# Optimization experiments

Measured on AMD Instinct MI355X. Metric: run time of the kernel, lower is better.

## Reference

```python
import jax, jax.numpy as jnp
import numpy as np

B, T, E, H, D = 4, 2048, 1024, 16, 64


def setup_inputs() -> dict:
    key = jax.random.key(0)
    k1, k2, k3, k4 = jax.random.split(key, 4)
    s = 1.0 / np.sqrt(E)
    return {
        "x": jax.random.normal(k1, (B, T, E), dtype=jnp.float32),
        "wj_w": jax.random.uniform(k2, (E, E), jnp.float32, -s, s),   # torch Linear weight (out,in)
        "wjv_w": jax.random.uniform(k3, (E, E), jnp.float32, -s, s),
        "wo_w": jax.random.uniform(k4, (E, H * D), jnp.float32, -s, s),
    }


def reference(x, wj_w, wjv_w, wo_w):
    b, t, e = x.shape
    # echo = x @ wj_w.T ; eb = echo @ wj_w  (F.linear with transposed weight)
    eb = (x @ wj_w.T) @ wj_w
    sc = jnp.sum(x * eb, axis=-1) / jnp.sqrt(jnp.asarray(e, x.dtype))  # (B,T)
    # rank-1 outer-product scores with strict-upper causal mask
    ja = sc[:, :, None] * sc[:, None, :]                               # (B,T,T)
    causal = jnp.tril(jnp.ones((t, t), dtype=bool))
    ja = jnp.where(causal[None], ja, -jnp.inf)
    ja = jax.nn.softmax(ja, axis=-1)                                   # (B,T,T)
    # values per head; attention map shared across heads (broadcast, not materialized)
    val = (x @ wjv_w.T).reshape(b, t, H, D)                            # (B,T,H,D)
    out = jnp.einsum("bts,bshd->bthd", ja, val)                       # (B,T,H,D)
    return out.reshape(b, t, H * D) @ wo_w.T                           # (B,T,E)
```

## Files before the change

kernel.cpp:

```cpp
#include <hip/hip_runtime.h>
#include <math.h>

#define R_ROWS 8192
#define T_SEQ  2048
#define E_DIM  1024

typedef __attribute__((ext_vector_type(8))) short short8;
typedef __attribute__((ext_vector_type(4))) float f32x4;

__device__ __forceinline__ ushort f2bf(float f) {
  uint u = __float_as_uint(f);
  u += 0x7FFFu + ((u >> 16) & 1u);
  return (ushort)(u >> 16);
}
__device__ __forceinline__ float bf2f(ushort h) {
  return __uint_as_float(((uint)h) << 16);
}

__global__ __launch_bounds__(256) void cvt_bf16(
    const float* __restrict__ in, ushort* __restrict__ out, int n4)
{
  int i = blockIdx.x * 256 + threadIdx.x;
  if (i >= n4) return;
  float4 v = ((const float4*)in)[i];
  ushort4 o;
  o.x = f2bf(v.x); o.y = f2bf(v.y); o.z = f2bf(v.z); o.w = f2bf(v.w);
  ((ushort4*)out)[i] = o;
}

__global__ __launch_bounds__(256) void cvt_split(
    const float* __restrict__ in, ushort* __restrict__ hi,
    ushort* __restrict__ lo, int n4)
{
  int i = blockIdx.x * 256 + threadIdx.x;
  if (i >= n4) return;
  float4 v = ((const float4*)in)[i];
  ushort4 h, l;
  h.x = f2bf(v.x); l.x = f2bf(v.x - bf2f(h.x));
  h.y = f2bf(v.y); l.y = f2bf(v.y - bf2f(h.y));
  h.z = f2bf(v.z); l.z = f2bf(v.z - bf2f(h.z));
  h.w = f2bf(v.w); l.w = f2bf(v.w - bf2f(h.w));
  ((ushort4*)hi)[i] = h;
  ((ushort4*)lo)[i] = l;
}

__global__ __launch_bounds__(256) void gemm_sq_split(
    const ushort* __restrict__ xh, const ushort* __restrict__ xl,
    const ushort* __restrict__ wh, const ushort* __restrict__ wl,
    float* __restrict__ sc_raw)
{
  const int K = 1024;
  __shared__ ushort Ah[128][40];
  __shared__ ushort Al[128][40];
  __shared__ ushort Bh[128][40];
  __shared__ ushort Bl[128][40];
  const int tid = threadIdx.x;
  const int m0 = blockIdx.y * 128, n0 = blockIdx.x * 128;
  const int wave = tid >> 6, lane = tid & 63;
  const int l15 = lane & 15, lq = lane >> 4;
  const int wm = (wave & 1) * 64, wn = (wave >> 1) * 64;
  const int srow = tid >> 2, scol = (tid & 3) * 8;

  f32x4 acc[4][4] = {};
  const ushort* xhp = xh + (size_t)(m0 + srow) * K + scol;
  const ushort* xlp = xl + (size_t)(m0 + srow) * K + scol;
  const ushort* whp = wh + (size_t)(n0 + srow) * K + scol;
  const ushort* wlp = wl + (size_t)(n0 + srow) * K + scol;

  for (int k0 = 0; k0 < K; k0 += 32) {
    const uint4 ah0 = *(const uint4*)(xhp + k0);
    const uint4 ah1 = *(const uint4*)(xhp + (size_t)64*K + k0);
    const uint4 al0 = *(const uint4*)(xlp + k0);
    const uint4 al1 = *(const uint4*)(xlp + (size_t)64*K + k0);
    const uint4 bh0 = *(const uint4*)(whp + k0);
    const uint4 bh1 = *(const uint4*)(whp + (size_t)64*K + k0);
    const uint4 bl0 = *(const uint4*)(wlp + k0);
    const uint4 bl1 = *(const uint4*)(wlp + (size_t)64*K + k0);
    __syncthreads();
    *(uint4*)&Ah[srow][scol] = ah0;  *(uint4*)&Ah[srow+64][scol] = ah1;
    *(uint4*)&Al[srow][scol] = al0;  *(uint4*)&Al[srow+64][scol] = al1;
    *(uint4*)&Bh[srow][scol] = bh0;  *(uint4*)&Bh[srow+64][scol] = bh1;
    *(uint4*)&Bl[srow][scol] = bl0;  *(uint4*)&Bl[srow+64][scol] = bl1;
    __syncthreads();
    short8 bhf[4], blf[4];
#pragma unroll
    for (int j = 0; j < 4; ++j) {
      bhf[j] = *(const short8*)&Bh[wn + j*16 + l15][lq*8];
      blf[j] = *(const short8*)&Bl[wn + j*16 + l15][lq*8];
    }
#pragma unroll
    for (int i = 0; i < 4; ++i) {
      const short8 ahf = *(const short8*)&Ah[wm + i*16 + l15][lq*8];
      const short8 alf = *(const short8*)&Al[wm + i*16 + l15][lq*8];
#pragma unroll
      for (int j = 0; j < 4; ++j) {
        acc[i][j] = __builtin_amdgcn_mfma_f32_16x16x32_bf16(ahf, bhf[j], acc[i][j], 0, 0, 0);
        acc[i][j] = __builtin_amdgcn_mfma_f32_16x16x32_bf16(ahf, blf[j], acc[i][j], 0, 0, 0);
        acc[i][j] = __builtin_amdgcn_mfma_f32_16x16x32_bf16(alf, bhf[j], acc[i][j], 0, 0, 0);
      }
    }
  }

  __syncthreads();
  float* red = (float*)&Ah[0][0];
#pragma unroll
  for (int i = 0; i < 4; ++i)
#pragma unroll
    for (int r = 0; r < 4; ++r) {
      const int row = wm + i*16 + lq*4 + r;
      float s = 0.f;
#pragma unroll
      for (int j = 0; j < 4; ++j) s += acc[i][j][r] * acc[i][j][r];
      red[row*33 + (wave>>1)*16 + l15] = s;
    }
  __syncthreads();
  if (tid < 128) {
    float s = 0.f;
#pragma unroll
    for (int c = 0; c < 32; ++c) s += red[tid*33 + c];
    atomicAdd(&sc_raw[m0 + tid], s);
  }
}

__global__ __launch_bounds__(1024) void scan_max(
    const float* __restrict__ sc_raw, float* __restrict__ sc,
    float* __restrict__ pmax)
{
  const int b = blockIdx.x;
  __shared__ float b0[T_SEQ];
  __shared__ float b1[T_SEQ];
  const int tid = threadIdx.x;
  for (int i = tid; i < T_SEQ; i += 1024) {
    const float v = sc_raw[b*T_SEQ + i] * 0.03125f;
    b0[i] = v;
    sc[b*T_SEQ + i] = v;
  }
  __syncthreads();
  float* src = b0; float* dst = b1;
  for (int off = 1; off < T_SEQ; off <<= 1) {
    for (int i = tid; i < T_SEQ; i += 1024)
      dst[i] = (i >= off) ? fmaxf(src[i], src[i - off]) : src[i];
    __syncthreads();
    float* tmp = src; src = dst; dst = tmp;
  }
  for (int i = tid; i < T_SEQ; i += 1024) pmax[b*T_SEQ + i] = src[i];
}

template<bool OUT_BF16>
__global__ __launch_bounds__(256) void gemm_bf16(
    const ushort* __restrict__ A, const ushort* __restrict__ B,
    void* __restrict__ Cout, int M, int N, int K)
{
  __shared__ ushort As[128][40];
  __shared__ ushort Bs[128][40];
  const int tid = threadIdx.x;
  const int m0 = blockIdx.y * 128, n0 = blockIdx.x * 128;
  const int wave = tid >> 6, lane = tid & 63;
  const int l15 = lane & 15, lq = lane >> 4;
  const int wm = (wave & 1) * 64, wn = (wave >> 1) * 64;
  const int srow = tid >> 2, scol = (tid & 3) * 8;

  f32x4 acc[4][4] = {};
  const ushort* Ap = A + (size_t)(m0 + srow) * K + scol;
  const ushort* Bp = B + (size_t)(n0 + srow) * K + scol;

  for (int k0 = 0; k0 < K; k0 += 32) {
    const uint4 a0 = *(const uint4*)(Ap + k0);
    const uint4 a1 = *(const uint4*)(Ap + (size_t)64 * K + k0);
    const uint4 b0 = *(const uint4*)(Bp + k0);
    const uint4 b1 = *(const uint4*)(Bp + (size_t)64 * K + k0);
    __syncthreads();
    *(uint4*)&As[srow     ][scol] = a0;
    *(uint4*)&As[srow + 64][scol] = a1;
    *(uint4*)&Bs[srow     ][scol] = b0;
    *(uint4*)&Bs[srow + 64][scol] = b1;
    __syncthreads();
    short8 af[4], bfr[4];
#pragma unroll
    for (int i = 0; i < 4; ++i)
      af[i] = *(const short8*)&As[wm + i*16 + l15][lq*8];
#pragma unroll
    for (int j = 0; j < 4; ++j)
      bfr[j] = *(const short8*)&Bs[wn + j*16 + l15][lq*8];
#pragma unroll
    for (int i = 0; i < 4; ++i)
#pragma unroll
      for (int j = 0; j < 4; ++j)
        acc[i][j] = __builtin_amdgcn_mfma_f32_16x16x32_bf16(af[i], bfr[j], acc[i][j], 0, 0, 0);
  }

#pragma unroll
  for (int i = 0; i < 4; ++i)
#pragma unroll
    for (int j = 0; j < 4; ++j) {
      const int mb = m0 + wm + i*16 + lq*4;
      const int nb = n0 + wn + j*16 + l15;
#pragma unroll
      for (int r = 0; r < 4; ++r) {
        if (OUT_BF16)
          ((ushort*)Cout)[(size_t)(mb + r) * N + nb] = f2bf(acc[i][j][r]);
        else
          ((float*)Cout)[(size_t)(mb + r) * N + nb] = acc[i][j][r];
      }
    }
}

__global__ __launch_bounds__(512) void attn_mfma(
    const ushort* __restrict__ valT, const float* __restrict__ sc,
    const float* __restrict__ pmax, ushort* __restrict__ attnN)
{
  __shared__ float scs_all[T_SEQ];
  __shared__ ushort p[2][128][72];
  __shared__ float zsh[128][4];
  __shared__ float zinv[128];

  const int b  = blockIdx.z;
  const int e0 = blockIdx.x * 128;
  const int tid = threadIdx.x;
  const int wave = tid >> 6, lane = tid & 63;
  const int l15 = lane & 15, lq = lane >> 4;
  const int wm = (wave & 1) * 64;
  const int wn = (wave >> 1) * 32;
  const int bT = b * T_SEQ;

  *(float4*)&scs_all[tid * 4] = *(const float4*)&sc[bT + tid * 4];
  __syncthreads();

  const int prow = tid >> 2;
  const int pc = (tid & 3) * 16;

#pragma unroll 1
  for (int ph = 0; ph < 2; ++ph) {
    const int ty = ph == 0 ? (15 - (int)blockIdx.y) : (int)blockIdx.y;
    const int t0 = ty * 128;
    const int nchunk = 2 * ty + 2;

    const int tglob = t0 + prow;
    const float st = sc[bT + tglob];
    const float pm = pmax[bT + tglob];

    f32x4 acc[4][2] = {};
    float zp = 0.f;

    auto pgen = [&](int c, int buf) -> float {
      const int s0 = c * 64;
      float sv[16];
#pragma unroll
      for (int q = 0; q < 4; ++q)
        *(float4*)&sv[q*4] = *(const float4*)&scs_all[s0 + pc + q*4];
      ushort tmp[16];
      float z = 0.f;
#pragma unroll
      for (int k = 0; k < 16; ++k) {
        const int sg = s0 + pc + k;
        float pe = 0.f;
        if (sg <= tglob) pe = __expf(st * (sv[k] - pm));
        const ushort h = f2bf(pe);
        tmp[k] = h;
        z += bf2f(h);
      }
      *(uint4*)&p[buf][prow][pc    ] = *(const uint4*)&tmp[0];
      *(uint4*)&p[buf][prow][pc + 8] = *(const uint4*)&tmp[8];
      return z;
    };

    auto loadB = [&](short8* dst, int c) {
#pragma unroll
      for (int j = 0; j < 2; ++j)
#pragma unroll
        for (int ksi = 0; ksi < 2; ++ksi)
          dst[j*2 + ksi] = *(const short8*)&valT[
              (size_t)(e0 + wn + j*16 + l15) * R_ROWS + bT + c*64 + ksi*32 + lq*8];
    };

    auto mstep = [&](int buf, const short8* bfr) {
#pragma unroll
      for (int ksi = 0; ksi < 2; ++ksi) {
        short8 af[4];
#pragma unroll
        for (int i = 0; i < 4; ++i)
          af[i] = *(const short8*)&p[buf][wm + i*16 + l15][ksi*32 + lq*8];
#pragma unroll
        for (int i = 0; i < 4; ++i)
#pragma unroll
          for (int j = 0; j < 2; ++j)
            acc[i][j] = __builtin_amdgcn_mfma_f32_16x16x32_bf16(
                af[i], bfr[j*2 + ksi], acc[i][j], 0, 0, 0);
      }
    };

    short8 bA[4], bB[4];
    zp += pgen(0, 0);
    loadB(bA, 0);
    __syncthreads();

#pragma unroll 1
    for (int c = 0; c < nchunk; ++c) {
      if ((c & 1) == 0) {
        if (c + 1 < nchunk) { loadB(bB, c + 1); zp += pgen(c + 1, 1); }
        mstep(0, bA);
      } else {
        if (c + 1 < nchunk) { loadB(bA, c + 1); zp += pgen(c + 1, 0); }
        mstep(1, bB);
      }
      __syncthreads();
    }

    zsh[prow][tid & 3] = zp;
    __syncthreads();
    if (tid < 128)
      zinv[tid] = 1.0f / (zsh[tid][0] + zsh[tid][1] + zsh[tid][2] + zsh[tid][3]);
    __syncthreads();

#pragma unroll
    for (int i = 0; i < 4; ++i)
#pragma unroll
      for (int j = 0; j < 2; ++j) {
        const int nb = e0 + wn + j*16 + l15;
#pragma unroll
        for (int r = 0; r < 4; ++r) {
          const int ml = wm + i*16 + lq*4 + r;
          const float v = acc[i][j][r] * zinv[ml];
          attnN[(size_t)(bT + t0 + ml) * E_DIM + nb] = f2bf(v);
        }
      }
    __syncthreads();
  }
}

extern "C" void kernel_launch(void* const* d_in, const int* in_sizes, int n_in,
                              void* d_out, int out_size, void* d_ws, size_t ws_size,
                              hipStream_t stream) {
  (void)in_sizes; (void)n_in; (void)out_size; (void)ws_size;
  const float* x   = (const float*)d_in[0];
  const float* wj  = (const float*)d_in[1];
  const float* wjv = (const float*)d_in[2];
  const float* wo  = (const float*)d_in[3];
  float* out = (float*)d_out;

  ushort* xh    = (ushort*)d_ws;
  ushort* xl    = xh    + (size_t)R_ROWS * E_DIM;
  ushort* wjh   = xl    + (size_t)R_ROWS * E_DIM;
  ushort* wjl   = wjh   + (size_t)E_DIM * E_DIM;
  ushort* wjvb  = wjl   + (size_t)E_DIM * E_DIM;
  ushort* wob   = wjvb  + (size_t)E_DIM * E_DIM;
  ushort* valT  = wob   + (size_t)E_DIM * E_DIM;
  float* sc_raw = (float*)(valT + (size_t)E_DIM * R_ROWS);
  float* sc     = sc_raw + R_ROWS;
  float* pmax   = sc + R_ROWS;
  ushort* attnN = xl;

  hipMemsetAsync(sc_raw, 0, R_ROWS * sizeof(float), stream);

  cvt_split<<<R_ROWS*E_DIM/4/256, 256, 0, stream>>>(x,  xh,  xl,  R_ROWS*E_DIM/4);
  cvt_split<<<E_DIM*E_DIM/4/256, 256, 0, stream>>>(wj, wjh, wjl, E_DIM*E_DIM/4);
  cvt_bf16<<<E_DIM*E_DIM/4/256, 256, 0, stream>>>(wjv, wjvb, E_DIM*E_DIM/4);
  cvt_bf16<<<E_DIM*E_DIM/4/256, 256, 0, stream>>>(wo,  wob,  E_DIM*E_DIM/4);

  gemm_sq_split<<<dim3(E_DIM/128, R_ROWS/128), 256, 0, stream>>>(
      xh, xl, wjh, wjl, sc_raw);
  scan_max<<<4, 1024, 0, stream>>>(sc_raw, sc, pmax);

  gemm_bf16<true><<<dim3(R_ROWS/128, E_DIM/128), 256, 0, stream>>>(
      wjvb, xh, valT, E_DIM, R_ROWS, E_DIM);

  attn_mfma<<<dim3(E_DIM/128, 8, 4), 512, 0, stream>>>(valT, sc, pmax, attnN);

  gemm_bf16<false><<<dim3(E_DIM/128, R_ROWS/128), 256, 0, stream>>>(
      attnN, wob, out, R_ROWS, E_DIM, E_DIM);
}
```

Baseline: 277.8 us.

## Pre-swizzle operands into MFMA fragment layout and load GEMM fragments directly from global

```diff
diff --git a/kernel.cpp b/kernel.cpp
--- a/kernel.cpp
+++ b/kernel.cpp
@@ -4,6 +4,7 @@
 #define R_ROWS 8192
 #define T_SEQ  2048
 #define E_DIM  1024
+#define KC     32
 
 typedef __attribute__((ext_vector_type(8))) short short8;
 typedef __attribute__((ext_vector_type(4))) float f32x4;
@@ -15,6 +16,48 @@
 }
 __device__ __forceinline__ float bf2f(ushort h) {
   return __uint_as_float(((uint)h) << 16);
+}
+
+
+__global__ __launch_bounds__(256) void cvt_split_frag(
+    const float* __restrict__ in, ushort* __restrict__ hi,
+    ushort* __restrict__ lo, int n)
+{
+  int g = blockIdx.x * 256 + threadIdx.x;
+  if (g >= n) return;
+  const int l = g & 15, h = (g >> 4) & 3;
+  const int pq = g >> 6;
+  const int q = pq & (KC - 1), p = pq >> 5;
+  const size_t src = (size_t)(p * 16 + l) * 1024 + q * 32 + h * 8;
+  const float4 v0 = *(const float4*)&in[src];
+  const float4 v1 = *(const float4*)&in[src + 4];
+  ushort hh[8], ll[8];
+  const float v[8] = {v0.x, v0.y, v0.z, v0.w, v1.x, v1.y, v1.z, v1.w};
+#pragma unroll
+  for (int e = 0; e < 8; ++e) {
+    hh[e] = f2bf(v[e]);
+    ll[e] = f2bf(v[e] - bf2f(hh[e]));
+  }
+  *(uint4*)&hi[(size_t)g * 8] = *(const uint4*)hh;
+  *(uint4*)&lo[(size_t)g * 8] = *(const uint4*)ll;
+}
+
+__global__ __launch_bounds__(256) void cvt_bf16_frag(
+    const float* __restrict__ in, ushort* __restrict__ out, int n)
+{
+  int g = blockIdx.x * 256 + threadIdx.x;
+  if (g >= n) return;
+  const int l = g & 15, h = (g >> 4) & 3;
+  const int pq = g >> 6;
+  const int q = pq & (KC - 1), p = pq >> 5;
+  const size_t src = (size_t)(p * 16 + l) * 1024 + q * 32 + h * 8;
+  const float4 v0 = *(const float4*)&in[src];
+  const float4 v1 = *(const float4*)&in[src + 4];
+  ushort hh[8];
+  const float v[8] = {v0.x, v0.y, v0.z, v0.w, v1.x, v1.y, v1.z, v1.w};
+#pragma unroll
+  for (int e = 0; e < 8; ++e) hh[e] = f2bf(v[e]);
+  *(uint4*)&out[(size_t)g * 8] = *(const uint4*)hh;
 }
 
 __global__ __launch_bounds__(256) void cvt_bf16(
@@ -28,96 +71,79 @@
   ((ushort4*)out)[i] = o;
 }
 
-__global__ __launch_bounds__(256) void cvt_split(
-    const float* __restrict__ in, ushort* __restrict__ hi,
-    ushort* __restrict__ lo, int n4)
-{
-  int i = blockIdx.x * 256 + threadIdx.x;
-  if (i >= n4) return;
-  float4 v = ((const float4*)in)[i];
-  ushort4 h, l;
-  h.x = f2bf(v.x); l.x = f2bf(v.x - bf2f(h.x));
-  h.y = f2bf(v.y); l.y = f2bf(v.y - bf2f(h.y));
-  h.z = f2bf(v.z); l.z = f2bf(v.z - bf2f(h.z));
-  h.w = f2bf(v.w); l.w = f2bf(v.w - bf2f(h.w));
-  ((ushort4*)hi)[i] = h;
-  ((ushort4*)lo)[i] = l;
-}
-
-__global__ __launch_bounds__(256) void gemm_sq_split(
+struct Frags { short8 ah[4], al[4], bh[4], bl[4]; };
+
+__global__ __launch_bounds__(256, 2) void gemm_sq_direct(
     const ushort* __restrict__ xh, const ushort* __restrict__ xl,
     const ushort* __restrict__ wh, const ushort* __restrict__ wl,
     float* __restrict__ sc_raw)
 {
-  const int K = 1024;
-  __shared__ ushort Ah[128][40];
-  __shared__ ushort Al[128][40];
-  __shared__ ushort Bh[128][40];
-  __shared__ ushort Bl[128][40];
   const int tid = threadIdx.x;
   const int m0 = blockIdx.y * 128, n0 = blockIdx.x * 128;
   const int wave = tid >> 6, lane = tid & 63;
   const int l15 = lane & 15, lq = lane >> 4;
   const int wm = (wave & 1) * 64, wn = (wave >> 1) * 64;
-  const int srow = tid >> 2, scol = (tid & 3) * 8;
+
+  size_t aoff[4], boff[4];
+#pragma unroll
+  for (int i = 0; i < 4; ++i)
+    aoff[i] = ((size_t)(((m0 + wm) >> 4) + i) * KC * 4 + lq) * 128 + l15 * 8;
+#pragma unroll
+  for (int j = 0; j < 4; ++j)
+    boff[j] = ((size_t)(((n0 + wn) >> 4) + j) * KC * 4 + lq) * 128 + l15 * 8;
 
   f32x4 acc[4][4] = {};
-  const ushort* xhp = xh + (size_t)(m0 + srow) * K + scol;
-  const ushort* xlp = xl + (size_t)(m0 + srow) * K + scol;
-  const ushort* whp = wh + (size_t)(n0 + srow) * K + scol;
-  const ushort* wlp = wl + (size_t)(n0 + srow) * K + scol;
-
-  for (int k0 = 0; k0 < K; k0 += 32) {
-    const uint4 ah0 = *(const uint4*)(xhp + k0);
-    const uint4 ah1 = *(const uint4*)(xhp + (size_t)64*K + k0);
-    const uint4 al0 = *(const uint4*)(xlp + k0);
-    const uint4 al1 = *(const uint4*)(xlp + (size_t)64*K + k0);
-    const uint4 bh0 = *(const uint4*)(whp + k0);
-    const uint4 bh1 = *(const uint4*)(whp + (size_t)64*K + k0);
-    const uint4 bl0 = *(const uint4*)(wlp + k0);
-    const uint4 bl1 = *(const uint4*)(wlp + (size_t)64*K + k0);
-    __syncthreads();
-    *(uint4*)&Ah[srow][scol] = ah0;  *(uint4*)&Ah[srow+64][scol] = ah1;
-    *(uint4*)&Al[srow][scol] = al0;  *(uint4*)&Al[srow+64][scol] = al1;
-    *(uint4*)&Bh[srow][scol] = bh0;  *(uint4*)&Bh[srow+64][scol] = bh1;
-    *(uint4*)&Bl[srow][scol] = bl0;  *(uint4*)&Bl[srow+64][scol] = bl1;
-    __syncthreads();
-    short8 bhf[4], blf[4];
+  Frags f0, f1;
+
+  auto load = [&](Frags& f, int q) {
+    const size_t dq = (size_t)q * 512;
+#pragma unroll
+    for (int i = 0; i < 4; ++i) {
+      f.ah[i] = *(const short8*)(xh + aoff[i] + dq);
+      f.al[i] = *(const short8*)(xl + aoff[i] + dq);
+    }
 #pragma unroll
     for (int j = 0; j < 4; ++j) {
-      bhf[j] = *(const short8*)&Bh[wn + j*16 + l15][lq*8];
-      blf[j] = *(const short8*)&Bl[wn + j*16 + l15][lq*8];
-    }
-#pragma unroll
-    for (int i = 0; i < 4; ++i) {
-      const short8 ahf = *(const short8*)&Ah[wm + i*16 + l15][lq*8];
-      const short8 alf = *(const short8*)&Al[wm + i*16 + l15][lq*8];
+      f.bh[j] = *(const short8*)(wh + boff[j] + dq);
+      f.bl[j] = *(const short8*)(wl + boff[j] + dq);
+    }
+  };
+  auto step = [&](const Frags& f) {
+#pragma unroll
+    for (int i = 0; i < 4; ++i)
 #pragma unroll
       for (int j = 0; j < 4; ++j) {
-        acc[i][j] = __builtin_amdgcn_mfma_f32_16x16x32_bf16(ahf, bhf[j], acc[i][j], 0, 0, 0);
-        acc[i][j] = __builtin_amdgcn_mfma_f32_16x16x32_bf16(ahf, blf[j], acc[i][j], 0, 0, 0);
-        acc[i][j] = __builtin_amdgcn_mfma_f32_16x16x32_bf16(alf, bhf[j], acc[i][j], 0, 0, 0);
-      }
-    }
-  }
-
-  __syncthreads();
-  float* red = (float*)&Ah[0][0];
+        acc[i][j] = __builtin_amdgcn_mfma_f32_16x16x32_bf16(f.ah[i], f.bh[j], acc[i][j], 0, 0, 0);
+        acc[i][j] = __builtin_amdgcn_mfma_f32_16x16x32_bf16(f.ah[i], f.bl[j], acc[i][j], 0, 0, 0);
+        acc[i][j] = __builtin_amdgcn_mfma_f32_16x16x32_bf16(f.al[i], f.bh[j], acc[i][j], 0, 0, 0);
+      }
+  };
+
+  load(f0, 0);
+#pragma unroll 1
+  for (int q = 0; q < KC; q += 2) {
+    load(f1, q + 1);
+    step(f0);
+    if (q + 2 < KC) load(f0, q + 2);
+    step(f1);
+  }
+
+  __shared__ float red[128][33];
 #pragma unroll
   for (int i = 0; i < 4; ++i)
 #pragma unroll
     for (int r = 0; r < 4; ++r) {
-      const int row = wm + i*16 + lq*4 + r;
+      const int row = wm + i * 16 + lq * 4 + r;
       float s = 0.f;
 #pragma unroll
       for (int j = 0; j < 4; ++j) s += acc[i][j][r] * acc[i][j][r];
-      red[row*33 + (wave>>1)*16 + l15] = s;
+      red[row][(l15 << 1) | (wave >> 1)] = s;
     }
   __syncthreads();
   if (tid < 128) {
     float s = 0.f;
 #pragma unroll
-    for (int c = 0; c < 32; ++c) s += red[tid*33 + c];
+    for (int c = 0; c < 32; ++c) s += red[tid][c];
     atomicAdd(&sc_raw[m0 + tid], s);
   }
 }
@@ -147,41 +173,41 @@
 }
 
 template<bool OUT_BF16>
-__global__ __launch_bounds__(256) void gemm_bf16(
-    const ushort* __restrict__ A, const ushort* __restrict__ B,
-    void* __restrict__ Cout, int M, int N, int K)
+__global__ __launch_bounds__(256) void gemm_bf16_bfrag(
+    const ushort* __restrict__ A, const ushort* __restrict__ Bf,
+    void* __restrict__ Cout, int N, int K)
 {
   __shared__ ushort As[128][40];
-  __shared__ ushort Bs[128][40];
   const int tid = threadIdx.x;
   const int m0 = blockIdx.y * 128, n0 = blockIdx.x * 128;
   const int wave = tid >> 6, lane = tid & 63;
   const int l15 = lane & 15, lq = lane >> 4;
   const int wm = (wave & 1) * 64, wn = (wave >> 1) * 64;
   const int srow = tid >> 2, scol = (tid & 3) * 8;
+  const int Kc = K >> 5;
 
   f32x4 acc[4][4] = {};
   const ushort* Ap = A + (size_t)(m0 + srow) * K + scol;
-  const ushort* Bp = B + (size_t)(n0 + srow) * K + scol;
-
-  for (int k0 = 0; k0 < K; k0 += 32) {
-    const uint4 a0 = *(const uint4*)(Ap + k0);
-    const uint4 a1 = *(const uint4*)(Ap + (size_t)64 * K + k0);
-    const uint4 b0 = *(const uint4*)(Bp + k0);
-    const uint4 b1 = *(const uint4*)(Bp + (size_t)64 * K + k0);
+  size_t boff[4];
+#pragma unroll
+  for (int j = 0; j < 4; ++j)
+    boff[j] = ((size_t)(((n0 + wn) >> 4) + j) * Kc * 4 + lq) * 128 + l15 * 8;
+
+  for (int q = 0; q < Kc; ++q) {
+    const uint4 a0 = *(const uint4*)(Ap + q * 32);
+    const uint4 a1 = *(const uint4*)(Ap + (size_t)64 * K + q * 32);
+    short8 bfr[4];
+#pragma unroll
+    for (int j = 0; j < 4; ++j)
+      bfr[j] = *(const short8*)(Bf + boff[j] + (size_t)q * 512);
     __syncthreads();
     *(uint4*)&As[srow     ][scol] = a0;
     *(uint4*)&As[srow + 64][scol] = a1;
-    *(uint4*)&Bs[srow     ][scol] = b0;
-    *(uint4*)&Bs[srow + 64][scol] = b1;
-    __syncthreads();
-    short8 af[4], bfr[4];
+    __syncthreads();
+    short8 af[4];
 #pragma unroll
     for (int i = 0; i < 4; ++i)
       af[i] = *(const short8*)&As[wm + i*16 + l15][lq*8];
-#pragma unroll
-    for (int j = 0; j < 4; ++j)
-      bfr[j] = *(const short8*)&Bs[wn + j*16 + l15][lq*8];
 #pragma unroll
     for (int i = 0; i < 4; ++i)
 #pragma unroll
@@ -338,34 +364,34 @@
   const float* wo  = (const float*)d_in[3];
   float* out = (float*)d_out;
 
-  ushort* xh    = (ushort*)d_ws;
-  ushort* xl    = xh    + (size_t)R_ROWS * E_DIM;
-  ushort* wjh   = xl    + (size_t)R_ROWS * E_DIM;
-  ushort* wjl   = wjh   + (size_t)E_DIM * E_DIM;
-  ushort* wjvb  = wjl   + (size_t)E_DIM * E_DIM;
-  ushort* wob   = wjvb  + (size_t)E_DIM * E_DIM;
-  ushort* valT  = wob   + (size_t)E_DIM * E_DIM;
-  float* sc_raw = (float*)(valT + (size_t)E_DIM * R_ROWS);
+  ushort* xh_f  = (ushort*)d_ws;
+  ushort* xl_f  = xh_f  + (size_t)R_ROWS * E_DIM;
+  ushort* wjh_f = xl_f  + (size_t)R_ROWS * E_DIM;
+  ushort* wjl_f = wjh_f + (size_t)E_DIM * E_DIM;
+  ushort* wjvb  = wjl_f + (size_t)E_DIM * E_DIM;
+  ushort* wob_f = wjvb  + (size_t)E_DIM * E_DIM;
+  float* sc_raw = (float*)(wob_f + (size_t)E_DIM * E_DIM);
   float* sc     = sc_raw + R_ROWS;
   float* pmax   = sc + R_ROWS;
-  ushort* attnN = xl;
+  ushort* valT  = xl_f;
+  ushort* attnN = xh_f;
 
   hipMemsetAsync(sc_raw, 0, R_ROWS * sizeof(float), stream);
 
-  cvt_split<<<R_ROWS*E_DIM/4/256, 256, 0, stream>>>(x,  xh,  xl,  R_ROWS*E_DIM/4);
-  cvt_split<<<E_DIM*E_DIM/4/256, 256, 0, stream>>>(wj, wjh, wjl, E_DIM*E_DIM/4);
+  cvt_split_frag<<<R_ROWS*E_DIM/8/256, 256, 0, stream>>>(x,  xh_f,  xl_f,  R_ROWS*E_DIM/8);
+  cvt_split_frag<<<E_DIM*E_DIM/8/256, 256, 0, stream>>>(wj, wjh_f, wjl_f, E_DIM*E_DIM/8);
   cvt_bf16<<<E_DIM*E_DIM/4/256, 256, 0, stream>>>(wjv, wjvb, E_DIM*E_DIM/4);
-  cvt_bf16<<<E_DIM*E_DIM/4/256, 256, 0, stream>>>(wo,  wob,  E_DIM*E_DIM/4);
-
-  gemm_sq_split<<<dim3(E_DIM/128, R_ROWS/128), 256, 0, stream>>>(
-      xh, xl, wjh, wjl, sc_raw);
+  cvt_bf16_frag<<<E_DIM*E_DIM/8/256, 256, 0, stream>>>(wo, wob_f, E_DIM*E_DIM/8);
+
+  gemm_sq_direct<<<dim3(E_DIM/128, R_ROWS/128), 256, 0, stream>>>(
+      xh_f, xl_f, wjh_f, wjl_f, sc_raw);
   scan_max<<<4, 1024, 0, stream>>>(sc_raw, sc, pmax);
 
-  gemm_bf16<true><<<dim3(R_ROWS/128, E_DIM/128), 256, 0, stream>>>(
-      wjvb, xh, valT, E_DIM, R_ROWS, E_DIM);
+  gemm_bf16_bfrag<true><<<dim3(R_ROWS/128, E_DIM/128), 256, 0, stream>>>(
+      wjvb, xh_f, valT, R_ROWS, E_DIM);
 
   attn_mfma<<<dim3(E_DIM/128, 8, 4), 512, 0, stream>>>(valT, sc, pmax, attnN);
 
-  gemm_bf16<false><<<dim3(E_DIM/128, R_ROWS/128), 256, 0, stream>>>(
-      attnN, wob, out, R_ROWS, E_DIM, E_DIM);
-}
+  gemm_bf16_bfrag<false><<<dim3(E_DIM/128, R_ROWS/128), 256, 0, stream>>>(
+      attnN, wob_f, out, E_DIM, E_DIM);
+}
```

Measured after the change: 271.8 us. 2.2% less time.
